# Kernel optimization log

Hardware: AMD Instinct MI355X
Metric: run time of the kernel (lower is better)

The kernel has to match this reference:

```python
import jax, jax.numpy as jnp
import numpy as np

B, D, K = 32768, 256, 2048
BETA = 0.25


def setup_inputs() -> dict:
    key = jax.random.key(0)
    k1, k2 = jax.random.split(key)
    latents = jax.random.normal(k1, (B, D), dtype=jnp.float32)
    # nn.Embedding weight initialized uniform(-1/K, 1/K)
    embedding = jax.random.uniform(k2, (K, D), dtype=jnp.float32,
                                   minval=-1.0 / K, maxval=1.0 / K)
    return {"latents": latents, "embedding": embedding}


def reference(latents, embedding):
    # Squared-L2 distances: [B, K]
    dist = (jnp.sum(latents ** 2, axis=1, keepdims=True)
            + jnp.sum(embedding ** 2, axis=1)
            - 2.0 * jnp.matmul(latents, embedding.T))
    encoding_inds = jnp.argmin(dist, axis=1)  # [B]

    # Gather codebook rows (equivalent to one-hot @ embedding)
    quantized = embedding[encoding_inds]  # [B, D]

    commitment_loss = jnp.mean((jax.lax.stop_gradient(quantized) - latents) ** 2)
    embedding_loss = jnp.mean((quantized - jax.lax.stop_gradient(latents)) ** 2)
    vq_loss = commitment_loss * BETA + embedding_loss

    # Straight-through estimator
    quantized_st = latents + jax.lax.stop_gradient(quantized - latents)

    # avg_probs = mean of one-hot over batch == normalized histogram of inds
    counts = jnp.zeros((K,), dtype=jnp.float32).at[encoding_inds].add(1.0)
    avg_probs = counts / B
    entropy_vq = -jnp.sum(avg_probs * jnp.log(avg_probs + 1e-10))

    # dist values at selected codes
    cluster_metric = jnp.mean(
        jnp.take_along_axis(dist, encoding_inds[:, None], axis=1))

    return (quantized_st, vq_loss, entropy_vq,
            encoding_inds[:, None], cluster_metric)
```

## Files before the change

### kernel.cpp

```cpp
#include <hip/hip_runtime.h>
#include <math.h>

#define B_ROWS 32768
#define D_DIM  256
#define K_CODES 2048

#define OUT_Q   0
#define OUT_VQ  8388608
#define OUT_ENT 8388609
#define OUT_IND 8388610
#define OUT_CM  8421378


#define WS_SE2   0
#define WS_SX2   8192
#define WS_CNT   139264
#define WS_DMIN  147456
#define WS_INDS  278528
#define WS_MSEP  409600
#define WS_DISTP 475136
#define WS_BCAT  540672
#define WS_CS    3686400
#define WS_CK    5783552

typedef _Float16 f16x8 __attribute__((ext_vector_type(8)));
typedef float f32x4 __attribute__((ext_vector_type(4)));
typedef union { _Float16 h[4]; uint2 u2; } h4pack;

__global__ __launch_bounds__(256) void k_convA(const float* __restrict__ X,
                                               _Float16* __restrict__ A,
                                               float* __restrict__ sx2) {
  int w = threadIdx.x >> 6, lane = threadIdx.x & 63;
  int row = blockIdx.x * 4 + w;
  float4 v = ((const float4*)(X + (size_t)row * D_DIM))[lane];
  float s = v.x * v.x + v.y * v.y + v.z * v.z + v.w * v.w;
#pragma unroll
  for (int off = 32; off > 0; off >>= 1) s += __shfl_xor(s, off, 64);
  if (lane == 0) sx2[row] = s;
  h4pack hi, lo;
  hi.h[0] = (_Float16)v.x; hi.h[1] = (_Float16)v.y;
  hi.h[2] = (_Float16)v.z; hi.h[3] = (_Float16)v.w;
  lo.h[0] = (_Float16)((v.x - (float)hi.h[0]) * 4096.0f);
  lo.h[1] = (_Float16)((v.y - (float)hi.h[1]) * 4096.0f);
  lo.h[2] = (_Float16)((v.z - (float)hi.h[2]) * 4096.0f);
  lo.h[3] = (_Float16)((v.w - (float)hi.h[3]) * 4096.0f);
  *(uint2*)&A[(size_t)row * 512 + 4 * lane] = hi.u2;
  *(uint2*)&A[(size_t)row * 512 + 256 + 4 * lane] = lo.u2;
}

__global__ __launch_bounds__(256) void k_convB(const float* __restrict__ E,
                                               _Float16* __restrict__ Bc,
                                               float* __restrict__ se2) {
  int w = threadIdx.x >> 6, lane = threadIdx.x & 63;
  int row = blockIdx.x * 4 + w;
  float4 v = ((const float4*)(E + (size_t)row * D_DIM))[lane];
  float s = v.x * v.x + v.y * v.y + v.z * v.z + v.w * v.w;
#pragma unroll
  for (int off = 32; off > 0; off >>= 1) s += __shfl_xor(s, off, 64);
  if (lane == 0) se2[row] = s;
  const float S = 4194304.0f;
  const float SH = 0.000244140625f;
  float e0 = v.x * S, e1 = v.y * S, e2 = v.z * S, e3 = v.w * S;
  h4pack b1, b2, b3;
  b1.h[0] = (_Float16)e0; b1.h[1] = (_Float16)e1;
  b1.h[2] = (_Float16)e2; b1.h[3] = (_Float16)e3;
  b2.h[0] = (_Float16)((float)b1.h[0] * SH);
  b2.h[1] = (_Float16)((float)b1.h[1] * SH);
  b2.h[2] = (_Float16)((float)b1.h[2] * SH);
  b2.h[3] = (_Float16)((float)b1.h[3] * SH);
  b3.h[0] = (_Float16)(e0 - (float)b1.h[0]);
  b3.h[1] = (_Float16)(e1 - (float)b1.h[1]);
  b3.h[2] = (_Float16)(e2 - (float)b1.h[2]);
  b3.h[3] = (_Float16)(e3 - (float)b1.h[3]);
  *(uint2*)&Bc[(size_t)row * 768 + 4 * lane] = b1.u2;
  *(uint2*)&Bc[(size_t)row * 768 + 256 + 4 * lane] = b2.u2;
  *(uint2*)&Bc[(size_t)row * 768 + 512 + 4 * lane] = b3.u2;
}

__global__ __launch_bounds__(256, 3) void k_mfma(
    const _Float16* __restrict__ A, const _Float16* __restrict__ Bc,
    const float* __restrict__ se2, const float* __restrict__ sx2,
    float* __restrict__ cs, int* __restrict__ ck) {
  __shared__ _Float16 As[128 * 32];
  __shared__ _Float16 Bs[128 * 32];
  __shared__ float sxs[128], ses[128];
  __shared__ float sred[2][128];
  __shared__ int ired[2][128];
  const int tid = threadIdx.x;
  const int w = tid >> 6, lane = tid & 63;
  const int rowblk = blockIdx.x >> 4, colblk = blockIdx.x & 15;
  const int row0 = rowblk * 128, col0 = colblk * 128;
  const int lr = lane >> 2, lc = lane & 3;
  const int q = lane >> 4, c = lane & 15;
  const int wr = (w >> 1) * 64, wc = (w & 1) * 64;

  if (tid < 128) { sxs[tid] = sx2[row0 + tid]; ses[tid] = se2[col0 + tid]; }

  f32x4 acc[4][4];
#pragma unroll
  for (int i = 0; i < 4; i++)
#pragma unroll
    for (int j = 0; j < 4; j++) acc[i][j] = (f32x4){0.f, 0.f, 0.f, 0.f};

  for (int kt = 0; kt < 24; ++kt) {
    int a_off = (kt < 8) ? kt * 64 : (kt < 16) ? 512 + (kt - 8) * 64
                                               : (kt - 16) * 64;
    int b_off = kt * 64;
    __syncthreads();
#pragma unroll
    for (int t = 0; t < 2; ++t) {
      int s = w * 2 + t;
      const char* ga = (const char*)A +
          (((size_t)(row0 + s * 16 + lr)) << 10) + a_off + lc * 16;
      const char* gb = (const char*)Bc +
          ((size_t)(col0 + s * 16 + lr)) * 1536 + b_off + lc * 16;
      __builtin_amdgcn_global_load_lds(
          (const __attribute__((address_space(1))) unsigned int*)ga,
          (__attribute__((address_space(3))) unsigned int*)((char*)As + s * 1024),
          16, 0, 0);
      __builtin_amdgcn_global_load_lds(
          (const __attribute__((address_space(1))) unsigned int*)gb,
          (__attribute__((address_space(3))) unsigned int*)((char*)Bs + s * 1024),
          16, 0, 0);
    }
    __builtin_amdgcn_s_waitcnt(0x0f70);
    __syncthreads();
    f16x8 af[4], bf[4];
#pragma unroll
    for (int i = 0; i < 4; ++i) {
      af[i] = *(const f16x8*)&As[(wr + i * 16 + c) * 32 + q * 8];
      bf[i] = *(const f16x8*)&Bs[(wc + i * 16 + c) * 32 + q * 8];
    }
#pragma unroll
    for (int i = 0; i < 4; ++i)
#pragma unroll
      for (int j = 0; j < 4; ++j)
        acc[i][j] =
            __builtin_amdgcn_mfma_f32_16x16x32_f16(af[i], bf[j], acc[i][j], 0, 0, 0);
  }

  const float inv = 4.76837158203125e-07f;
#pragma unroll
  for (int i = 0; i < 4; ++i) {
#pragma unroll
    for (int r = 0; r < 4; ++r) {
      int lrow = wr + i * 16 + q * 4 + r;
      float sx = sxs[lrow];
      float bs = 3.402823466e38f;
      int bk = 0;
#pragma unroll
      for (int j = 0; j < 4; ++j) {
        int nloc = wc + j * 16 + c;
        float t1 = sx + ses[nloc];
        float d = t1 - acc[i][j][r] * inv;
        if (d < bs) { bs = d; bk = col0 + nloc; }
      }
#pragma unroll
      for (int off = 1; off < 16; off <<= 1) {
        float os = __shfl_xor(bs, off, 64);
        int ok = __shfl_xor(bk, off, 64);
        if (os < bs || (os == bs && ok < bk)) { bs = os; bk = ok; }
      }
      if (c == 0) { sred[w & 1][lrow] = bs; ired[w & 1][lrow] = bk; }
    }
  }
  __syncthreads();
  if (tid < 128) {
    float s0 = sred[0][tid]; int k0 = ired[0][tid];
    float s1 = sred[1][tid]; int k1 = ired[1][tid];
    if (s1 < s0) { s0 = s1; k0 = k1; }
    cs[colblk * B_ROWS + row0 + tid] = s0;
    ck[colblk * B_ROWS + row0 + tid] = k0;
  }
}

__global__ __launch_bounds__(256) void k_merge(
    const float* __restrict__ cs, const int* __restrict__ ck,
    float* __restrict__ out_ind, int* __restrict__ inds,
    float* __restrict__ dmin, int* __restrict__ counts) {
  int r = blockIdx.x * 256 + threadIdx.x;
  float bs = cs[r];
  int bk = ck[r];
#pragma unroll
  for (int t = 1; t < 16; t++) {
    float s = cs[t * B_ROWS + r];
    int k = ck[t * B_ROWS + r];
    if (s < bs) { bs = s; bk = k; }
  }
  out_ind[r] = (float)bk;
  inds[r] = bk;
  dmin[r] = bs;
  atomicAdd(&counts[bk], 1);
}

__global__ __launch_bounds__(256) void k_gather(
    const float* __restrict__ X, const float* __restrict__ E,
    const int* __restrict__ inds, const float* __restrict__ dmin,
    float* __restrict__ outq, double* __restrict__ msep,
    double* __restrict__ distp) {
  int wave = threadIdx.x >> 6, lane = threadIdx.x & 63;
  double msum = 0.0;
  double dsum = 0.0;
#pragma unroll
  for (int rr = 0; rr < 4; rr++) {
    int b = blockIdx.x * 16 + wave * 4 + rr;
    int ind = inds[b];
    float4 x4 = ((const float4*)(X + (size_t)b * D_DIM))[lane];
    float4 q4 = ((const float4*)(E + (size_t)ind * D_DIM))[lane];
    float d0 = q4.x - x4.x, d1 = q4.y - x4.y, d2 = q4.z - x4.z, d3 = q4.w - x4.w;
    float4 o;
    o.x = x4.x + d0; o.y = x4.y + d1; o.z = x4.z + d2; o.w = x4.w + d3;
    ((float4*)(outq + (size_t)b * D_DIM))[lane] = o;
    float v = d0 * d0 + d1 * d1 + d2 * d2 + d3 * d3;
#pragma unroll
    for (int off = 32; off > 0; off >>= 1) v += __shfl_xor(v, off, 64);
    if (lane == 0) { msum += (double)v; dsum += (double)dmin[b]; }
  }
  if (lane == 0) {
    int w = blockIdx.x * 4 + wave;
    msep[w] = msum;
    distp[w] = dsum;
  }
}

__global__ __launch_bounds__(256) void k_final(
    const int* __restrict__ counts, const double* __restrict__ msep,
    const double* __restrict__ distp, float* __restrict__ out) {
  __shared__ double red[256];
  int t = threadIdx.x;

  double m = 0.0;
  for (int i = t; i < 8192; i += 256) m += msep[i];
  red[t] = m;
  __syncthreads();
  for (int s = 128; s > 0; s >>= 1) {
    if (t < s) red[t] += red[t + s];
    __syncthreads();
  }
  if (t == 0) {
    double mse = red[0] / ((double)B_ROWS * (double)D_DIM);
    out[OUT_VQ] = (float)(mse * 1.25);
  }
  __syncthreads();

  double d = 0.0;
  for (int i = t; i < 8192; i += 256) d += distp[i];
  red[t] = d;
  __syncthreads();
  for (int s = 128; s > 0; s >>= 1) {
    if (t < s) red[t] += red[t + s];
    __syncthreads();
  }
  if (t == 0) out[OUT_CM] = (float)(red[0] / (double)B_ROWS);
  __syncthreads();

  double e = 0.0;
  for (int k = t; k < K_CODES; k += 256) {
    float p = (float)counts[k] * (1.0f / 32768.0f);
    e += (double)(p * logf(p + 1e-10f));
  }
  red[t] = e;
  __syncthreads();
  for (int s = 128; s > 0; s >>= 1) {
    if (t < s) red[t] += red[t + s];
    __syncthreads();
  }
  if (t == 0) out[OUT_ENT] = (float)(-red[0]);
}

extern "C" void kernel_launch(void* const* d_in, const int* in_sizes, int n_in,
                              void* d_out, int out_size, void* d_ws,
                              size_t ws_size, hipStream_t stream) {
  const float* X = (const float*)d_in[0];
  const float* E = (const float*)d_in[1];
  float* out = (float*)d_out;
  char* ws = (char*)d_ws;
  float* se2 = (float*)(ws + WS_SE2);
  float* sx2 = (float*)(ws + WS_SX2);
  int* counts = (int*)(ws + WS_CNT);
  float* dmin = (float*)(ws + WS_DMIN);
  int* inds = (int*)(ws + WS_INDS);
  double* msep = (double*)(ws + WS_MSEP);
  double* distp = (double*)(ws + WS_DISTP);
  _Float16* Bcat = (_Float16*)(ws + WS_BCAT);
  float* cs = (float*)(ws + WS_CS);
  int* ckp = (int*)(ws + WS_CK);
  _Float16* Acat = (_Float16*)d_out;

  hipMemsetAsync(counts, 0, K_CODES * sizeof(int), stream);
  k_convA<<<B_ROWS / 4, 256, 0, stream>>>(X, Acat, sx2);
  k_convB<<<K_CODES / 4, 256, 0, stream>>>(E, Bcat, se2);
  k_mfma<<<(B_ROWS / 128) * (K_CODES / 128), 256, 0, stream>>>(
      Acat, Bcat, se2, sx2, cs, ckp);
  k_merge<<<B_ROWS / 256, 256, 0, stream>>>(cs, ckp, out + OUT_IND, inds, dmin,
                                            counts);
  k_gather<<<B_ROWS / 16, 256, 0, stream>>>(X, E, inds, dmin, out + OUT_Q,
                                            msep, distp);
  k_final<<<1, 256, 0, stream>>>(counts, msep, distp, out);
}
```

Measured before the change: 279.6 us.

## Double-buffer MFMA tiles, merge argmin via packed atomicMin, drop merge kernel

```diff
diff --git a/kernel.cpp b/kernel.cpp
--- a/kernel.cpp
+++ b/kernel.cpp
@@ -15,13 +15,10 @@
 #define WS_SE2   0
 #define WS_SX2   8192
 #define WS_CNT   139264
-#define WS_DMIN  147456
-#define WS_INDS  278528
+#define WS_PACK  147456
 #define WS_MSEP  409600
 #define WS_DISTP 475136
 #define WS_BCAT  540672
-#define WS_CS    3686400
-#define WS_CK    5783552
 
 typedef _Float16 f16x8 __attribute__((ext_vector_type(8)));
 typedef float f32x4 __attribute__((ext_vector_type(4)));
@@ -77,134 +74,141 @@
   *(uint2*)&Bc[(size_t)row * 768 + 512 + 4 * lane] = b3.u2;
 }
 
-__global__ __launch_bounds__(256, 3) void k_mfma(
+__global__ __launch_bounds__(256, 4) void k_mfma(
     const _Float16* __restrict__ A, const _Float16* __restrict__ Bc,
     const float* __restrict__ se2, const float* __restrict__ sx2,
-    float* __restrict__ cs, int* __restrict__ ck) {
-  __shared__ _Float16 As[128 * 32];
-  __shared__ _Float16 Bs[128 * 32];
-  __shared__ float sxs[128], ses[128];
-  __shared__ float sred[2][128];
-  __shared__ int ired[2][128];
+    unsigned long long* __restrict__ packed) {
+  __shared__ _Float16 As[2][128 * 32];
+  __shared__ _Float16 Bs[2][128 * 32];
+  __shared__ float sxs[128];
   const int tid = threadIdx.x;
   const int w = tid >> 6, lane = tid & 63;
-  const int rowblk = blockIdx.x >> 4, colblk = blockIdx.x & 15;
-  const int row0 = rowblk * 128, col0 = colblk * 128;
+  const int rowblk = blockIdx.x & 255, cg = blockIdx.x >> 8;
+  const int row0 = rowblk * 128, col00 = cg * 512;
   const int lr = lane >> 2, lc = lane & 3;
   const int q = lane >> 4, c = lane & 15;
   const int wr = (w >> 1) * 64, wc = (w & 1) * 64;
 
-  if (tid < 128) { sxs[tid] = sx2[row0 + tid]; ses[tid] = se2[col0 + tid]; }
-
-  f32x4 acc[4][4];
-#pragma unroll
-  for (int i = 0; i < 4; i++)
-#pragma unroll
-    for (int j = 0; j < 4; j++) acc[i][j] = (f32x4){0.f, 0.f, 0.f, 0.f};
-
-  for (int kt = 0; kt < 24; ++kt) {
-    int a_off = (kt < 8) ? kt * 64 : (kt < 16) ? 512 + (kt - 8) * 64
-                                               : (kt - 16) * 64;
-    int b_off = kt * 64;
-    __syncthreads();
+  if (tid < 128) sxs[tid] = sx2[row0 + tid];
+
+  const char* Abase = (const char*)A;
+  const char* Bbase = (const char*)Bc;
+
+  auto issue = [&](int ct_i, int ktl_i, int bsel) {
+    int a_off = (ktl_i < 8) ? ktl_i * 64
+              : (ktl_i < 16) ? 512 + (ktl_i - 8) * 64 : (ktl_i - 16) * 64;
+    int b_off = ktl_i * 64;
+    int colb = col00 + ct_i * 128;
 #pragma unroll
     for (int t = 0; t < 2; ++t) {
       int s = w * 2 + t;
-      const char* ga = (const char*)A +
-          (((size_t)(row0 + s * 16 + lr)) << 10) + a_off + lc * 16;
-      const char* gb = (const char*)Bc +
-          ((size_t)(col0 + s * 16 + lr)) * 1536 + b_off + lc * 16;
+      const char* ga =
+          Abase + (((size_t)(row0 + s * 16 + lr)) << 10) + a_off + lc * 16;
+      const char* gb =
+          Bbase + ((size_t)(colb + s * 16 + lr)) * 1536 + b_off + lc * 16;
       __builtin_amdgcn_global_load_lds(
           (const __attribute__((address_space(1))) unsigned int*)ga,
-          (__attribute__((address_space(3))) unsigned int*)((char*)As + s * 1024),
+          (__attribute__((address_space(3))) unsigned int*)((char*)&As[bsel][0] +
+                                                            s * 1024),
           16, 0, 0);
       __builtin_amdgcn_global_load_lds(
           (const __attribute__((address_space(1))) unsigned int*)gb,
-          (__attribute__((address_space(3))) unsigned int*)((char*)Bs + s * 1024),
+          (__attribute__((address_space(3))) unsigned int*)((char*)&Bs[bsel][0] +
+                                                            s * 1024),
           16, 0, 0);
     }
-    __builtin_amdgcn_s_waitcnt(0x0f70);
-    __syncthreads();
-    f16x8 af[4], bf[4];
+  };
+
+  issue(0, 0, 0);
+
+  const float inv = 4.76837158203125e-07f;
+  for (int ct = 0; ct < 4; ++ct) {
+    f32x4 acc[4][4];
+#pragma unroll
+    for (int i = 0; i < 4; i++)
+#pragma unroll
+      for (int j = 0; j < 4; j++) acc[i][j] = (f32x4){0.f, 0.f, 0.f, 0.f};
+
+#pragma unroll 2
+    for (int ktl = 0; ktl < 24; ++ktl) {
+      __syncthreads();
+      int gidx = ct * 24 + ktl + 1;
+      if (gidx < 96) issue(gidx / 24, gidx % 24, (ktl + 1) & 1);
+      const int b = ktl & 1;
+      f16x8 af[4], bf[4];
+#pragma unroll
+      for (int i = 0; i < 4; ++i) {
+        af[i] = *(const f16x8*)&As[b][(wr + i * 16 + c) * 32 + q * 8];
+        bf[i] = *(const f16x8*)&Bs[b][(wc + i * 16 + c) * 32 + q * 8];
+      }
+#pragma unroll
+      for (int i = 0; i < 4; ++i)
+#pragma unroll
+        for (int j = 0; j < 4; ++j)
+          acc[i][j] = __builtin_amdgcn_mfma_f32_16x16x32_f16(af[i], bf[j],
+                                                             acc[i][j], 0, 0, 0);
+    }
+
+    int colb = col00 + ct * 128;
+    float se_j[4];
+#pragma unroll
+    for (int j = 0; j < 4; ++j) se_j[j] = se2[colb + wc + j * 16 + c];
 #pragma unroll
     for (int i = 0; i < 4; ++i) {
-      af[i] = *(const f16x8*)&As[(wr + i * 16 + c) * 32 + q * 8];
-      bf[i] = *(const f16x8*)&Bs[(wc + i * 16 + c) * 32 + q * 8];
+#pragma unroll
+      for (int r = 0; r < 4; ++r) {
+        int lrow = wr + i * 16 + q * 4 + r;
+        float sx = sxs[lrow];
+        float bs = 3.402823466e38f;
+        int bk = 0;
+#pragma unroll
+        for (int j = 0; j < 4; ++j) {
+          float t1 = sx + se_j[j];
+          float d = t1 - acc[i][j][r] * inv;
+          if (d < bs) { bs = d; bk = colb + wc + j * 16 + c; }
+        }
+#pragma unroll
+        for (int off = 1; off < 16; off <<= 1) {
+          float os = __shfl_xor(bs, off, 64);
+          int ok = __shfl_xor(bk, off, 64);
+          if (os < bs || (os == bs && ok < bk)) { bs = os; bk = ok; }
+        }
+        if (c == 0) {
+          unsigned long long v =
+              ((unsigned long long)__float_as_uint(bs) << 32) |
+              (unsigned long long)(unsigned int)bk;
+          atomicMin(&packed[row0 + lrow], v);
+        }
+      }
     }
-#pragma unroll
-    for (int i = 0; i < 4; ++i)
-#pragma unroll
-      for (int j = 0; j < 4; ++j)
-        acc[i][j] =
-            __builtin_amdgcn_mfma_f32_16x16x32_f16(af[i], bf[j], acc[i][j], 0, 0, 0);
-  }
-
-  const float inv = 4.76837158203125e-07f;
-#pragma unroll
-  for (int i = 0; i < 4; ++i) {
-#pragma unroll
-    for (int r = 0; r < 4; ++r) {
-      int lrow = wr + i * 16 + q * 4 + r;
-      float sx = sxs[lrow];
-      float bs = 3.402823466e38f;
-      int bk = 0;
-#pragma unroll
-      for (int j = 0; j < 4; ++j) {
-        int nloc = wc + j * 16 + c;
-        float t1 = sx + ses[nloc];
-        float d = t1 - acc[i][j][r] * inv;
-        if (d < bs) { bs = d; bk = col0 + nloc; }
-      }
-#pragma unroll
-      for (int off = 1; off < 16; off <<= 1) {
-        float os = __shfl_xor(bs, off, 64);
-        int ok = __shfl_xor(bk, off, 64);
-        if (os < bs || (os == bs && ok < bk)) { bs = os; bk = ok; }
-      }
-      if (c == 0) { sred[w & 1][lrow] = bs; ired[w & 1][lrow] = bk; }
-    }
-  }
-  __syncthreads();
-  if (tid < 128) {
-    float s0 = sred[0][tid]; int k0 = ired[0][tid];
-    float s1 = sred[1][tid]; int k1 = ired[1][tid];
-    if (s1 < s0) { s0 = s1; k0 = k1; }
-    cs[colblk * B_ROWS + row0 + tid] = s0;
-    ck[colblk * B_ROWS + row0 + tid] = k0;
-  }
-}
-
-__global__ __launch_bounds__(256) void k_merge(
-    const float* __restrict__ cs, const int* __restrict__ ck,
-    float* __restrict__ out_ind, int* __restrict__ inds,
-    float* __restrict__ dmin, int* __restrict__ counts) {
-  int r = blockIdx.x * 256 + threadIdx.x;
-  float bs = cs[r];
-  int bk = ck[r];
-#pragma unroll
-  for (int t = 1; t < 16; t++) {
-    float s = cs[t * B_ROWS + r];
-    int k = ck[t * B_ROWS + r];
-    if (s < bs) { bs = s; bk = k; }
-  }
-  out_ind[r] = (float)bk;
-  inds[r] = bk;
-  dmin[r] = bs;
-  atomicAdd(&counts[bk], 1);
+  }
 }
 
 __global__ __launch_bounds__(256) void k_gather(
     const float* __restrict__ X, const float* __restrict__ E,
-    const int* __restrict__ inds, const float* __restrict__ dmin,
-    float* __restrict__ outq, double* __restrict__ msep,
-    double* __restrict__ distp) {
-  int wave = threadIdx.x >> 6, lane = threadIdx.x & 63;
-  double msum = 0.0;
-  double dsum = 0.0;
+    const unsigned long long* __restrict__ packed, float* __restrict__ outq,
+    float* __restrict__ out_ind, int* __restrict__ counts,
+    double* __restrict__ msep, double* __restrict__ distp) {
+  __shared__ int sk[16];
+  __shared__ float sd[16];
+  int tid = threadIdx.x;
+  if (tid < 16) {
+    int row = blockIdx.x * 16 + tid;
+    unsigned long long v = packed[row];
+    int k = (int)(v & 0xFFFFFFFFull);
+    sk[tid] = k;
+    sd[tid] = __uint_as_float((unsigned int)(v >> 32));
+    out_ind[row] = (float)k;
+    atomicAdd(&counts[k], 1);
+  }
+  __syncthreads();
+  int wave = tid >> 6, lane = tid & 63;
+  double msum = 0.0, dsum = 0.0;
 #pragma unroll
   for (int rr = 0; rr < 4; rr++) {
-    int b = blockIdx.x * 16 + wave * 4 + rr;
-    int ind = inds[b];
+    int li = wave * 4 + rr;
+    int b = blockIdx.x * 16 + li;
+    int ind = sk[li];
     float4 x4 = ((const float4*)(X + (size_t)b * D_DIM))[lane];
     float4 q4 = ((const float4*)(E + (size_t)ind * D_DIM))[lane];
     float d0 = q4.x - x4.x, d1 = q4.y - x4.y, d2 = q4.z - x4.z, d3 = q4.w - x4.w;
@@ -214,12 +218,12 @@
     float v = d0 * d0 + d1 * d1 + d2 * d2 + d3 * d3;
 #pragma unroll
     for (int off = 32; off > 0; off >>= 1) v += __shfl_xor(v, off, 64);
-    if (lane == 0) { msum += (double)v; dsum += (double)dmin[b]; }
+    if (lane == 0) { msum += (double)v; dsum += (double)sd[li]; }
   }
   if (lane == 0) {
-    int w = blockIdx.x * 4 + wave;
-    msep[w] = msum;
-    distp[w] = dsum;
+    int wg = blockIdx.x * 4 + wave;
+    msep[wg] = msum;
+    distp[wg] = dsum;
   }
 }
 
@@ -278,23 +282,18 @@
   float* se2 = (float*)(ws + WS_SE2);
   float* sx2 = (float*)(ws + WS_SX2);
   int* counts = (int*)(ws + WS_CNT);
-  float* dmin = (float*)(ws + WS_DMIN);
-  int* inds = (int*)(ws + WS_INDS);
+  unsigned long long* packed = (unsigned long long*)(ws + WS_PACK);
   double* msep = (double*)(ws + WS_MSEP);
   double* distp = (double*)(ws + WS_DISTP);
   _Float16* Bcat = (_Float16*)(ws + WS_BCAT);
-  float* cs = (float*)(ws + WS_CS);
-  int* ckp = (int*)(ws + WS_CK);
   _Float16* Acat = (_Float16*)d_out;
 
   hipMemsetAsync(counts, 0, K_CODES * sizeof(int), stream);
+  hipMemsetAsync(packed, 0xFF, B_ROWS * sizeof(unsigned long long), stream);
   k_convA<<<B_ROWS / 4, 256, 0, stream>>>(X, Acat, sx2);
   k_convB<<<K_CODES / 4, 256, 0, stream>>>(E, Bcat, se2);
-  k_mfma<<<(B_ROWS / 128) * (K_CODES / 128), 256, 0, stream>>>(
-      Acat, Bcat, se2, sx2, cs, ckp);
-  k_merge<<<B_ROWS / 256, 256, 0, stream>>>(cs, ckp, out + OUT_IND, inds, dmin,
-                                            counts);
-  k_gather<<<B_ROWS / 16, 256, 0, stream>>>(X, E, inds, dmin, out + OUT_Q,
-                                            msep, distp);
+  k_mfma<<<1024, 256, 0, stream>>>(Acat, Bcat, se2, sx2, packed);
+  k_gather<<<B_ROWS / 16, 256, 0, stream>>>(X, E, packed, out + OUT_Q,
+                                            out + OUT_IND, counts, msep, distp);
   k_final<<<1, 256, 0, stream>>>(counts, msep, distp, out);
 }
```

Measured after the change: 277.0 us. No clear change (-0.9%).
